# Kernel optimization log

Hardware: AMD Instinct MI355X
Metric: run time of the kernel (lower is better)

Reference implementation:

```python
import jax, jax.numpy as jnp
import numpy as np

H_SPLITS = [2, 3, 3]          # crpe_window {3:2, 5:3, 7:3}
K_SIZES = [3, 5, 7]
NUM_HEADS = 8
EPS = 1e-6


def dwconv(x, w, b, k):
    # x: (B,C,H,W), w: (C,1,k,k) depthwise, 'same' padding
    y = jax.lax.conv_general_dilated(
        x, w, (1, 1), [(k // 2, k // 2)] * 2,
        feature_group_count=x.shape[1],
        dimension_numbers=('NCHW', 'OIHW', 'NCHW'))
    return y + b[None, :, None, None]


def layernorm(x, g, b):
    m = jnp.mean(x, -1, keepdims=True)
    v = jnp.var(x, -1, keepdims=True)
    return (x - m) * jax.lax.rsqrt(v + EPS) * g + b


def conv_rel_pos_enc(q, v, ws, bs, H, W):
    # ConvRelPosEnc (MPViT style, no cls token): q * depthwise_conv(v)
    B, h, N, Ch = q.shape
    v_img = v.transpose(0, 1, 3, 2).reshape(B, h * Ch, H, W)  # B (h Ch) H W
    splits = np.cumsum([hs * Ch for hs in H_SPLITS])[:-1]
    parts = jnp.split(v_img, splits, axis=1)
    conv_v = jnp.concatenate(
        [dwconv(p, w, b, k) for p, w, b, k in zip(parts, ws, bs, K_SIZES)], axis=1)
    conv_v = conv_v.reshape(B, h, Ch, N).transpose(0, 1, 3, 2)
    return q * conv_v


def setup_inputs() -> dict:
    key = jax.random.key(0)
    B, H, W, C, nd, r, mr = 8, 64, 64, 320, 4, 2, 4
    h = NUM_HEADS
    N = H * W
    Ch = C // h
    hid = C // r
    ks = jax.random.split(key, 16)
    s = 0.02
    return {
        'x': jax.random.normal(ks[0], (B, N, C), jnp.float32),
        'domain_label': jax.nn.one_hot(jax.random.randint(ks[1], (B,), 0, nd), nd, dtype=jnp.float32),
        'cpe_w': jax.random.normal(ks[2], (C, 1, 3, 3), jnp.float32) * s,
        'cpe_b': jnp.zeros((C,), jnp.float32),
        'ln1_g': jnp.ones((C,), jnp.float32), 'ln1_b': jnp.zeros((C,), jnp.float32),
        'qkv_w': jax.random.normal(ks[3], (3 * C, C), jnp.float32) * s,
        'qkv_b': jnp.zeros((3 * C,), jnp.float32),
        'crpe_w3': jax.random.normal(ks[4], (2 * Ch, 1, 3, 3), jnp.float32) * s,
        'crpe_b3': jnp.zeros((2 * Ch,), jnp.float32),
        'crpe_w5': jax.random.normal(ks[5], (3 * Ch, 1, 5, 5), jnp.float32) * s,
        'crpe_b5': jnp.zeros((3 * Ch,), jnp.float32),
        'crpe_w7': jax.random.normal(ks[6], (3 * Ch, 1, 7, 7), jnp.float32) * s,
        'crpe_b7': jnp.zeros((3 * Ch,), jnp.float32),
        'dom_w1': jax.random.normal(ks[7], (hid, nd), jnp.float32) * s,
        'dom_b1': jnp.zeros((hid,), jnp.float32),
        'dom_w2': jax.random.normal(ks[8], (C, hid), jnp.float32) * s,
        'dom_b2': jnp.zeros((C,), jnp.float32),
        'proj_w': jax.random.normal(ks[9], (C, C), jnp.float32) * s,
        'proj_b': jnp.zeros((C,), jnp.float32),
        'ln2_g': jnp.ones((C,), jnp.float32), 'ln2_b': jnp.zeros((C,), jnp.float32),
        'mlp_w1': jax.random.normal(ks[10], (mr * C, C), jnp.float32) * s,
        'mlp_b1': jnp.zeros((mr * C,), jnp.float32),
        'mlp_w2': jax.random.normal(ks[11], (C, mr * C), jnp.float32) * s,
        'mlp_b2': jnp.zeros((C,), jnp.float32),
        'H': H, 'W': W,
    }


def reference(x, domain_label, cpe_w, cpe_b, ln1_g, ln1_b, qkv_w, qkv_b,
              crpe_w3, crpe_b3, crpe_w5, crpe_b5, crpe_w7, crpe_b7,
              dom_w1, dom_b1, dom_w2, dom_b2, proj_w, proj_b,
              ln2_g, ln2_b, mlp_w1, mlp_b1, mlp_w2, mlp_b2, H, W):
    B, N, C = x.shape
    h = NUM_HEADS
    Ch = C // h
    scale = Ch ** -0.5
    # ConvPosEnc: depthwise 3x3 conv + residual
    img = x.transpose(0, 2, 1).reshape(B, C, H, W)
    x = (dwconv(img, cpe_w, cpe_b, 3) + img).reshape(B, C, N).transpose(0, 2, 1)
    # FactorAtt_ConvRelPosEnc_Sup
    cur = layernorm(x, ln1_g, ln1_b)
    qkv = (cur @ qkv_w.T + qkv_b).reshape(B, N, 3, h, Ch).transpose(2, 0, 3, 1, 4)
    q, k, v = qkv[0], qkv[1], qkv[2]          # (B,h,N,Ch) each
    k_sm = jax.nn.softmax(k, axis=2)          # softmax over tokens
    kv = jnp.einsum('bhnk,bhnv->bhkv', k_sm, v)   # (B,h,Ch,Ch)
    fa = jnp.einsum('bhnk,bhkv->bhnv', q, kv)
    fa = scale * fa + conv_rel_pos_enc(
        q, v, (crpe_w3, crpe_w5, crpe_w7), (crpe_b3, crpe_b5, crpe_b7), H, W)
    # domain gate: MLP(one_hot) -> softmax over heads, broadcast over tokens
    d = jax.nn.relu(domain_label @ dom_w1.T + dom_b1) @ dom_w2.T + dom_b2  # (B,C)
    d = jax.nn.softmax(d.reshape(B, h, 1, Ch), axis=1)
    att = (d * fa).transpose(0, 2, 1, 3).reshape(B, N, C)
    x = x + (att @ proj_w.T + proj_b)
    # MLP (GELU, ratio 4)
    cur = layernorm(x, ln2_g, ln2_b)
    cur = jax.nn.gelu(cur @ mlp_w1.T + mlp_b1, approximate=False) @ mlp_w2.T + mlp_b2
    return x + cur
```

## Files before the change

### kernel.cpp

```cpp
#include <hip/hip_runtime.h>
#include <hip/hip_bf16.h>
#include <math.h>
#include <type_traits>

#define B_    8
#define Nn    4096
#define Cc    320
#define QS    1024
#define ATT_SCALE 0.15811388300841897f

typedef __attribute__((ext_vector_type(8))) short s8v;
typedef __attribute__((ext_vector_type(4))) float f4v;

__device__ __forceinline__ float bf2f(short u) {
    return __uint_as_float(((unsigned int)(unsigned short)u) << 16);
}
__device__ __forceinline__ short f2bf(float f) {
    return (short)__bfloat16_as_ushort(__float2bfloat16(f));
}
__device__ __forceinline__ float gelu_fast(float v) {
    float u = v * (0.7978845608f + 0.0356774081f * v * v);
    float e = __expf(2.f * u);
    float t = 1.f - 2.f / (e + 1.f);
    return 0.5f * v * (1.f + t);
}

typedef const __attribute__((address_space(1))) unsigned int* gp1_t;
typedef __attribute__((address_space(3))) unsigned int* lp3_t;
__device__ __forceinline__ void gload16(const void* g, void* l) {
    __builtin_amdgcn_global_load_lds((gp1_t)g, (lp3_t)l, 16, 0, 0);
}

__global__ void cvt_all(const float* __restrict__ s0, const float* __restrict__ s1,
                        const float* __restrict__ s2, const float* __restrict__ s3,
                        __hip_bfloat16* __restrict__ d) {
    int i = blockIdx.x * 256 + threadIdx.x;
    if (i >= 1351680) return;
    const float* s; int j, rows, K;
    if (i < 327680)      { s = s0; j = i;          rows = 960;  K = 320; }
    else if (i < 450560) { s = s1; j = i - 327680; rows = 320;  K = 320; }
    else if (i < 860160) { s = s2; j = i - 450560; rows = 1280; K = 320; }
    else                 { s = s3; j = i - 860160; rows = 320;  K = 1280; }
    float v = (j / K < rows) ? s[j] : 0.f;
    d[i] = __float2bfloat16(v);
}

template<typename T>
__global__ void ln_kernel(const T* __restrict__ x, const float* __restrict__ g,
                          const float* __restrict__ bt, __hip_bfloat16* __restrict__ out) {
    int bn = blockIdx.x;
    int lane = threadIdx.x;
    const T* row = x + (size_t)bn * Cc;
    float v[5];
    float s = 0.f, s2 = 0.f;
    #pragma unroll
    for (int i = 0; i < 5; ++i) {
        if constexpr (std::is_same<T, float>::value) v[i] = row[lane + 64 * i];
        else v[i] = bf2f(((const short*)row)[lane + 64 * i]);
        s += v[i];
        s2 += v[i] * v[i];
    }
    #pragma unroll
    for (int off = 32; off > 0; off >>= 1) {
        s  += __shfl_down(s, off);
        s2 += __shfl_down(s2, off);
    }
    s  = __shfl(s, 0);
    s2 = __shfl(s2, 0);
    float mean = s * (1.f / 320.f);
    float var  = s2 * (1.f / 320.f) - mean * mean;
    float rstd = rsqrtf(var + 1e-6f);
    __hip_bfloat16* orow = out + (size_t)bn * Cc;
    #pragma unroll
    for (int i = 0; i < 5; ++i) {
        int c = lane + 64 * i;
        orow[c] = __float2bfloat16((v[i] - mean) * rstd * g[c] + bt[c]);
    }
}

template<int ACT, int RES, int WF32, int WBF16, int KT>
__global__ __launch_bounds__(512) void gemm_mfma(
        const __hip_bfloat16* __restrict__ A, const __hip_bfloat16* __restrict__ W,
        const float* __restrict__ bias, const void* __restrict__ resv,
        float* __restrict__ outf, __hip_bfloat16* __restrict__ outb,
        int NS, int Nreal) {
    __shared__ __align__(16) short As[256 * 64];
    __shared__ __align__(16) short Bs[128 * 64];
    int tid = threadIdx.x;
    int m0 = blockIdx.x << 8;
    int n0 = blockIdx.y << 7;
    int w = tid >> 6, lane = tid & 63;
    int wr = w >> 1, wc = w & 1;
    int lrow = lane & 15, lk = lane >> 4;
    f4v acc[4][4];
    #pragma unroll
    for (int i = 0; i < 4; ++i)
        #pragma unroll
        for (int j = 0; j < 4; ++j) acc[i][j] = (f4v){0.f, 0.f, 0.f, 0.f};

    int srow = (w << 3) + (lane >> 3);
    int slot = lane & 7;

    #pragma unroll
    for (int k0 = 0; k0 < KT; k0 += 64) {
        __syncthreads();
        #pragma unroll
        for (int i = 0; i < 4; ++i) {
            int row = i * 64 + srow;
            int sk = (slot ^ (row & 7)) << 3;
            gload16(&A[(size_t)(m0 + row) * KT + k0 + sk], &As[i * 4096 + w * 512]);
        }
        #pragma unroll
        for (int i = 0; i < 2; ++i) {
            int row = i * 64 + srow;
            int sk = (slot ^ (row & 7)) << 3;
            gload16(&W[(size_t)(n0 + row) * KT + k0 + sk], &Bs[i * 4096 + w * 512]);
        }
        __syncthreads();
        #pragma unroll
        for (int ks = 0; ks < 2; ++ks) {
            s8v af[4], bf[4];
            #pragma unroll
            for (int mi = 0; mi < 4; ++mi) {
                int row = wr * 64 + mi * 16 + lrow;
                int s = (ks * 4 + lk) ^ (row & 7);
                af[mi] = *reinterpret_cast<const s8v*>(&As[row * 64 + s * 8]);
            }
            #pragma unroll
            for (int ni = 0; ni < 4; ++ni) {
                int row = wc * 64 + ni * 16 + lrow;
                int s = (ks * 4 + lk) ^ (row & 7);
                bf[ni] = *reinterpret_cast<const s8v*>(&Bs[row * 64 + s * 8]);
            }
            #pragma unroll
            for (int mi = 0; mi < 4; ++mi)
                #pragma unroll
                for (int ni = 0; ni < 4; ++ni)
                    acc[mi][ni] = __builtin_amdgcn_mfma_f32_16x16x32_bf16(bf[ni], af[mi], acc[mi][ni], 0, 0, 0);
        }
    }
    #pragma unroll
    for (int mi = 0; mi < 4; ++mi) {
        int m = m0 + wr * 64 + mi * 16 + lrow;
        #pragma unroll
        for (int ni = 0; ni < 4; ++ni) {
            int n = n0 + wc * 64 + ni * 16 + (lk << 2);
            if (n >= Nreal) continue;
            f4v v4 = acc[mi][ni];
            float4 bv = *reinterpret_cast<const float4*>(&bias[n]);
            v4[0] += bv.x; v4[1] += bv.y; v4[2] += bv.z; v4[3] += bv.w;
            if (RES == 1) {
                const float* res = (const float*)resv;
                float4 rv = *reinterpret_cast<const float4*>(&res[(size_t)m * NS + n]);
                v4[0] += rv.x; v4[1] += rv.y; v4[2] += rv.z; v4[3] += rv.w;
            } else if (RES == 2) {
                const short* res = (const short*)resv;
                short4 rv = *reinterpret_cast<const short4*>(&res[(size_t)m * NS + n]);
                v4[0] += bf2f(rv.x); v4[1] += bf2f(rv.y);
                v4[2] += bf2f(rv.z); v4[3] += bf2f(rv.w);
            }
            if (ACT == 1) {
                #pragma unroll
                for (int r = 0; r < 4; ++r) v4[r] = gelu_fast(v4[r]);
            }
            if (WF32)
                *reinterpret_cast<float4*>(&outf[(size_t)m * NS + n]) =
                    make_float4(v4[0], v4[1], v4[2], v4[3]);
            if (WBF16) {
                ushort4 u;
                u.x = (unsigned short)f2bf(v4[0]);
                u.y = (unsigned short)f2bf(v4[1]);
                u.z = (unsigned short)f2bf(v4[2]);
                u.w = (unsigned short)f2bf(v4[3]);
                *reinterpret_cast<ushort4*>(&outb[(size_t)m * NS + n]) = u;
            }
        }
    }
}

template<int KSZ, int EPI, typename ST>
__global__ __launch_bounds__(256) void dwconv_tile(
        const ST* __restrict__ src, int sstride, int scoff,
        const float* __restrict__ wts, const float* __restrict__ bias, int cbase, int ngrp,
        const void* __restrict__ aux0v,
        const float* __restrict__ aux1,
        __hip_bfloat16* __restrict__ outb) {
    constexpr int P = KSZ / 2;
    constexpr int S = 16 + 2 * P;
    __shared__ float vt[S * S * 8];
    __shared__ float ws_[8 * KSZ * KSZ];
    int blk = blockIdx.x;
    int tile = blk & 15;
    int g  = (blk >> 4) % ngrp;
    int b  = (blk >> 4) / ngrp;
    int ty0 = (tile >> 2) << 4;
    int tx0 = (tile & 3) << 4;
    int c0 = cbase + g * 8;
    int tid = threadIdx.x;
    for (int e = tid; e < 8 * KSZ * KSZ; e += 256)
        ws_[e] = wts[g * 8 * KSZ * KSZ + e];
    const ST* sb = src + (size_t)b * Nn * sstride + scoff + c0;
    for (int e = tid; e < S * S; e += 256) {
        int hy = e / S, hx = e % S;
        int gy = ty0 - P + hy, gx = tx0 - P + hx;
        float px8[8];
        #pragma unroll
        for (int j = 0; j < 8; ++j) px8[j] = 0.f;
        if ((unsigned)gy < 64u && (unsigned)gx < 64u) {
            const ST* p = &sb[(size_t)((gy << 6) + gx) * sstride];
            if constexpr (std::is_same<ST, float>::value) {
                float4 lo = reinterpret_cast<const float4*>(p)[0];
                float4 hi = reinterpret_cast<const float4*>(p)[1];
                px8[0] = lo.x; px8[1] = lo.y; px8[2] = lo.z; px8[3] = lo.w;
                px8[4] = hi.x; px8[5] = hi.y; px8[6] = hi.z; px8[7] = hi.w;
            } else {
                s8v v8 = *reinterpret_cast<const s8v*>(p);
                #pragma unroll
                for (int j = 0; j < 8; ++j) px8[j] = bf2f(v8[j]);
            }
        }
        #pragma unroll
        for (int j = 0; j < 8; ++j) vt[e * 8 + j] = px8[j];
    }
    __syncthreads();
    int cl  = tid & 7;
    int px  = (tid >> 3) & 15;
    int pyh = tid >> 7;
    int c = c0 + cl;
    float acc[8];
    float bval = bias[g * 8 + cl];
    #pragma unroll
    for (int j = 0; j < 8; ++j) acc[j] = bval;
    #pragma unroll
    for (int dx = 0; dx < KSZ; ++dx) {
        float col[8 + KSZ - 1];
        #pragma unroll
        for (int i = 0; i < 8 + KSZ - 1; ++i)
            col[i] = vt[((pyh * 8 + i) * S + (px + dx)) * 8 + cl];
        #pragma unroll
        for (int j = 0; j < 8; ++j)
            #pragma unroll
            for (int dy = 0; dy < KSZ; ++dy)
                acc[j] += col[j + dy] * ws_[cl * KSZ * KSZ + dy * KSZ + dx];
    }
    #pragma unroll
    for (int j = 0; j < 8; ++j) {
        int n = ((ty0 + pyh * 8 + j) << 6) + tx0 + px;
        size_t bn = (size_t)b * Nn + n;
        if (EPI == 0) {
            float ctr = vt[((pyh * 8 + j + P) * S + (px + P)) * 8 + cl];
            outb[bn * Cc + c] = __float2bfloat16(acc[j] + ctr);
        } else {
            const short* fa0 = (const short*)aux0v;
            float qv  = bf2f(((const short*)src)[bn * (size_t)sstride + c]);
            float fav = bf2f(fa0[bn * Cc + c]);
            float r = aux1[(size_t)b * Cc + c] * (ATT_SCALE * fav + qv * acc[j]);
            outb[bn * Cc + c] = __float2bfloat16(r);
        }
    }
}

__global__ __launch_bounds__(256) void kv_mfma(const __hip_bfloat16* __restrict__ qkv,
                                               float* __restrict__ kvp) {
    __shared__ short lds[4 * 2 * 48 * 66];
    int blk = blockIdx.x;
    int s = blk & 7;
    int bh = blk >> 3;
    int h = bh & 7, b = bh >> 3;
    int tid = threadIdx.x;
    int w = tid >> 6, lane = tid & 63;
    short* ke_t = lds + w * 2 * 48 * 66;
    short* vv_t = ke_t + 48 * 66;
    for (int e = lane; e < 8 * 66; e += 64) {
        ke_t[40 * 66 + e] = 0;
        vv_t[40 * 66 + e] = 0;
    }
    for (int n = lane; n < 66; n += 64) vv_t[40 * 66 + n] = (short)0x3F80;

    const short* kb = (const short*)qkv + (size_t)b * Nn * QS + 320 + h * 40;
    const short* vb = kb + 320;
    int col0 = lane & 15, kq = lane >> 4;
    f4v acc[3][3];
    #pragma unroll
    for (int i = 0; i < 3; ++i)
        #pragma unroll
        for (int j = 0; j < 3; ++j) acc[i][j] = (f4v){0.f, 0.f, 0.f, 0.f};

    for (int t = w; t < 8; t += 4) {
        int n0 = s * 512 + t * 64;
        for (int e = lane; e < 320; e += 64) {
            int nl = e / 5, oct = e % 5;
            size_t go = (size_t)(n0 + nl) * QS + oct * 8;
            s8v k8 = *reinterpret_cast<const s8v*>(kb + go);
            s8v v8 = *reinterpret_cast<const s8v*>(vb + go);
            #pragma unroll
            for (int j = 0; j < 8; ++j) {
                ke_t[(oct * 8 + j) * 66 + nl] = f2bf(__expf(bf2f(k8[j])));
                vv_t[(oct * 8 + j) * 66 + nl] = v8[j];
            }
        }
        __syncthreads();
        #pragma unroll
        for (int ks = 0; ks < 2; ++ks) {
            s8v af[3], bfr[3];
            #pragma unroll
            for (int mt = 0; mt < 3; ++mt)
                af[mt] = *reinterpret_cast<const s8v*>(ke_t + (mt * 16 + col0) * 66 + ks * 32 + kq * 8);
            #pragma unroll
            for (int nt = 0; nt < 3; ++nt)
                bfr[nt] = *reinterpret_cast<const s8v*>(vv_t + (nt * 16 + col0) * 66 + ks * 32 + kq * 8);
            #pragma unroll
            for (int mt = 0; mt < 3; ++mt)
                #pragma unroll
                for (int nt = 0; nt < 3; ++nt)
                    acc[mt][nt] = __builtin_amdgcn_mfma_f32_16x16x32_bf16(af[mt], bfr[nt], acc[mt][nt], 0, 0, 0);
        }
        __syncthreads();
    }
    float* red = (float*)lds;
    #pragma unroll
    for (int mt = 0; mt < 3; ++mt) {
        #pragma unroll
        for (int nt = 0; nt < 3; ++nt) {
            #pragma unroll
            for (int r = 0; r < 4; ++r) {
                int ch = mt * 16 + kq * 4 + r;
                int cv = nt * 16 + col0;
                if (ch < 40) red[w * 1920 + ch * 48 + cv] = acc[mt][nt][r];
            }
        }
    }
    __syncthreads();
    for (int p = tid; p < 1920; p += 256) {
        float sv = red[p] + red[1920 + p] + red[2 * 1920 + p] + red[3 * 1920 + p];
        kvp[(size_t)blk * 1920 + p] = sv;
    }
}

__global__ void kv_combine2(const float* __restrict__ kvp, float* __restrict__ kv) {
    int bh = blockIdx.x;
    int tid = threadIdx.x;
    __shared__ float sinv[40];
    if (tid < 40) {
        float S = 0.f;
        for (int s2 = 0; s2 < 8; ++s2)
            S += kvp[(size_t)(bh * 8 + s2) * 1920 + tid * 48 + 40];
        sinv[tid] = 1.f / S;
    }
    __syncthreads();
    for (int p = tid; p < 1600; p += 256) {
        int ch = p / 40, cv = p % 40;
        float v = 0.f;
        for (int s2 = 0; s2 < 8; ++s2)
            v += kvp[(size_t)(bh * 8 + s2) * 1920 + ch * 48 + cv];
        kv[(size_t)bh * 1600 + p] = v * sinv[ch];
    }
}

__global__ void dgate_kernel(const float* __restrict__ lbl, const float* __restrict__ w1,
                             const float* __restrict__ b1, const float* __restrict__ w2,
                             const float* __restrict__ b2, float* __restrict__ dg) {
    int b = blockIdx.x;
    int tid = threadIdx.x;
    __shared__ float hid[160];
    __shared__ float dd[320];
    if (tid < 160) {
        float a = b1[tid];
        for (int d = 0; d < 4; ++d) a += w1[tid * 4 + d] * lbl[b * 4 + d];
        hid[tid] = fmaxf(a, 0.f);
    }
    __syncthreads();
    float a = b2[tid];
    for (int j = 0; j < 160; ++j) a += w2[tid * 160 + j] * hid[j];
    dd[tid] = a;
    __syncthreads();
    if (tid < 40) {
        float M = -1e30f;
        for (int h2 = 0; h2 < 8; ++h2) M = fmaxf(M, dd[h2 * 40 + tid]);
        float S = 0.f;
        float e[8];
        for (int h2 = 0; h2 < 8; ++h2) { e[h2] = __expf(dd[h2 * 40 + tid] - M); S += e[h2]; }
        float inv = 1.f / S;
        for (int h2 = 0; h2 < 8; ++h2) dg[b * 320 + h2 * 40 + tid] = e[h2] * inv;
    }
}

__global__ __launch_bounds__(256) void fa_kernel(const __hip_bfloat16* __restrict__ qkv,
        const float* __restrict__ kvmat, __hip_bfloat16* __restrict__ fa) {
    __shared__ float kvs[1600];
    int blk = blockIdx.x;
    int chunk = blk & 15;
    int bh = blk >> 4;
    int h = bh & 7, b = bh >> 3;
    int tid = threadIdx.x;
    for (int e = tid; e < 1600; e += 256) kvs[e] = kvmat[(size_t)bh * 1600 + e];
    __syncthreads();
    int n = chunk * 256 + tid;
    const short* qr = (const short*)qkv + (size_t)(b * Nn + n) * QS + h * 40;
    float q[40];
    #pragma unroll
    for (int i = 0; i < 5; ++i) {
        s8v v8 = reinterpret_cast<const s8v*>(qr)[i];
        #pragma unroll
        for (int j = 0; j < 8; ++j) q[i * 8 + j] = bf2f(v8[j]);
    }
    float o[40];
    #pragma unroll
    for (int cv = 0; cv < 40; ++cv) o[cv] = 0.f;
    #pragma unroll
    for (int ch = 0; ch < 40; ++ch) {
        float qv = q[ch];
        #pragma unroll
        for (int cv = 0; cv < 40; ++cv)
            o[cv] += qv * kvs[ch * 40 + cv];
    }
    short* fr = (short*)fa + (size_t)(b * Nn + n) * 320 + h * 40;
    #pragma unroll
    for (int i = 0; i < 5; ++i) {
        s8v u;
        #pragma unroll
        for (int j = 0; j < 8; ++j) u[j] = f2bf(o[i * 8 + j]);
        *reinterpret_cast<s8v*>(fr + i * 8) = u;
    }
}

extern "C" void kernel_launch(void* const* d_in, const int* in_sizes, int n_in,
                              void* d_out, int out_size, void* d_ws, size_t ws_size,
                              hipStream_t stream) {
    const float* x     = (const float*)d_in[0];
    const float* lbl   = (const float*)d_in[1];
    const float* cpe_w = (const float*)d_in[2];
    const float* cpe_b = (const float*)d_in[3];
    const float* ln1g  = (const float*)d_in[4];
    const float* ln1b  = (const float*)d_in[5];
    const float* qkv_w = (const float*)d_in[6];
    const float* qkv_b = (const float*)d_in[7];
    const float* w3    = (const float*)d_in[8];
    const float* b3    = (const float*)d_in[9];
    const float* w5    = (const float*)d_in[10];
    const float* b5    = (const float*)d_in[11];
    const float* w7    = (const float*)d_in[12];
    const float* b7    = (const float*)d_in[13];
    const float* dw1   = (const float*)d_in[14];
    const float* db1   = (const float*)d_in[15];
    const float* dw2   = (const float*)d_in[16];
    const float* db2   = (const float*)d_in[17];
    const float* pw    = (const float*)d_in[18];
    const float* pb    = (const float*)d_in[19];
    const float* ln2g  = (const float*)d_in[20];
    const float* ln2b  = (const float*)d_in[21];
    const float* m1w   = (const float*)d_in[22];
    const float* m1b   = (const float*)d_in[23];
    const float* m2w   = (const float*)d_in[24];
    const float* m2b   = (const float*)d_in[25];
    float* out = (float*)d_out;

    float* ws = (float*)d_ws;
    __hip_bfloat16* x1b  = (__hip_bfloat16*)ws; ws += 5242880;
    __hip_bfloat16* qkvb = (__hip_bfloat16*)ws; ws += 16777216;
    float* big  = ws; ws += 20971520;
    __hip_bfloat16* gelub = (__hip_bfloat16*)big;
    __hip_bfloat16* fab   = (__hip_bfloat16*)ws; ws += 5242880;
    __hip_bfloat16* bb1   = (__hip_bfloat16*)ws; ws += 5242880;
    __hip_bfloat16* wb    = (__hip_bfloat16*)ws; ws += 675840;
    float* kvp  = ws; ws += 983040;
    float* kv   = ws; ws += 102400;
    float* dg   = ws; ws += 2560;
    __hip_bfloat16* wbq  = wb;
    __hip_bfloat16* wbp  = wbq  + 1024 * 320;
    __hip_bfloat16* wbm1 = wbp  + 384 * 320;
    __hip_bfloat16* wbm2 = wbm1 + 1280 * 320;

    cvt_all<<<5280, 256, 0, stream>>>(qkv_w, pw, m1w, m2w, wb);
    dwconv_tile<3, 0, float><<<B_ * 40 * 16, 256, 0, stream>>>(
        x, 320, 0, cpe_w, cpe_b, 0, 40, nullptr, nullptr, x1b);
    ln_kernel<__hip_bfloat16><<<B_ * Nn, 64, 0, stream>>>(x1b, ln1g, ln1b, bb1);
    {
        dim3 g(128, 8);
        gemm_mfma<0, 0, 0, 1, 320><<<g, 512, 0, stream>>>(bb1, wbq, qkv_b, nullptr,
                                                          nullptr, qkvb, QS, 960);
    }
    kv_mfma<<<512, 256, 0, stream>>>(qkvb, kvp);
    kv_combine2<<<64, 256, 0, stream>>>(kvp, kv);
    dgate_kernel<<<B_, 320, 0, stream>>>(lbl, dw1, db1, dw2, db2, dg);
    fa_kernel<<<B_ * 8 * 16, 256, 0, stream>>>(qkvb, kv, fab);
    dwconv_tile<3, 1, __hip_bfloat16><<<B_ * 10 * 16, 256, 0, stream>>>(
        qkvb, QS, 640, w3, b3, 0, 10, fab, dg, bb1);
    dwconv_tile<5, 1, __hip_bfloat16><<<B_ * 15 * 16, 256, 0, stream>>>(
        qkvb, QS, 640, w5, b5, 80, 15, fab, dg, bb1);
    dwconv_tile<7, 1, __hip_bfloat16><<<B_ * 15 * 16, 256, 0, stream>>>(
        qkvb, QS, 640, w7, b7, 200, 15, fab, dg, bb1);
    {
        dim3 g(128, 3);
        gemm_mfma<0, 2, 1, 0, 320><<<g, 512, 0, stream>>>(bb1, wbp, pb, x1b,
                                                          out, nullptr, 320, 320);
    }
    ln_kernel<float><<<B_ * Nn, 64, 0, stream>>>(out, ln2g, ln2b, bb1);
    {
        dim3 g(128, 10);
        gemm_mfma<1, 0, 0, 1, 320><<<g, 512, 0, stream>>>(bb1, wbm1, m1b, nullptr,
                                                          nullptr, gelub, 1280, 1280);
    }
    {
        dim3 g(128, 3);
        gemm_mfma<0, 1, 1, 0, 1280><<<g, 512, 0, stream>>>(gelub, wbm2, m2b, out,
                                                           out, nullptr, 320, 320);
    }
}
```

Measured before the change: 315.3 us.

## Add full-N GEMM kernel for N=320 outputs and grouped block swizzle

Adds a gemm_fulln kernel with a 64-row by full-320-column tile for the projection and MLP2 GEMMs. This removes the padded 384-column tiling and the wasted third N-tile, and raises the block count to 512. The main GEMM now uses a 1D grid with a grouped swizzle (8 M-tiles per group) so that blocks sharing A tiles run close together for better L2 reuse. In exchange, the smaller M tile reuses each W load across fewer rows, and more of the W matrix is staged per block.

```diff
diff --git a/kernel.cpp b/kernel.cpp
--- a/kernel.cpp
+++ b/kernel.cpp
@@ -83,12 +83,15 @@
         const __hip_bfloat16* __restrict__ A, const __hip_bfloat16* __restrict__ W,
         const float* __restrict__ bias, const void* __restrict__ resv,
         float* __restrict__ outf, __hip_bfloat16* __restrict__ outb,
-        int NS, int Nreal) {
+        int NS, int Nreal, int gy) {
     __shared__ __align__(16) short As[256 * 64];
     __shared__ __align__(16) short Bs[128 * 64];
-    int tid = threadIdx.x;
-    int m0 = blockIdx.x << 8;
-    int n0 = blockIdx.y << 7;
+    int bid = blockIdx.x;
+    int grp8 = gy << 3;
+    int grp = bid / grp8, rem = bid % grp8;
+    int m0 = ((grp << 3) + (rem & 7)) << 8;
+    int n0 = (rem >> 3) << 7;
+    int tid = threadIdx.x;
     int w = tid >> 6, lane = tid & 63;
     int wr = w >> 1, wc = w & 1;
     int lrow = lane & 15, lk = lane >> 4;
@@ -146,6 +149,102 @@
         for (int ni = 0; ni < 4; ++ni) {
             int n = n0 + wc * 64 + ni * 16 + (lk << 2);
             if (n >= Nreal) continue;
+            f4v v4 = acc[mi][ni];
+            float4 bv = *reinterpret_cast<const float4*>(&bias[n]);
+            v4[0] += bv.x; v4[1] += bv.y; v4[2] += bv.z; v4[3] += bv.w;
+            if (RES == 1) {
+                const float* res = (const float*)resv;
+                float4 rv = *reinterpret_cast<const float4*>(&res[(size_t)m * NS + n]);
+                v4[0] += rv.x; v4[1] += rv.y; v4[2] += rv.z; v4[3] += rv.w;
+            } else if (RES == 2) {
+                const short* res = (const short*)resv;
+                short4 rv = *reinterpret_cast<const short4*>(&res[(size_t)m * NS + n]);
+                v4[0] += bf2f(rv.x); v4[1] += bf2f(rv.y);
+                v4[2] += bf2f(rv.z); v4[3] += bf2f(rv.w);
+            }
+            if (ACT == 1) {
+                #pragma unroll
+                for (int r = 0; r < 4; ++r) v4[r] = gelu_fast(v4[r]);
+            }
+            if (WF32)
+                *reinterpret_cast<float4*>(&outf[(size_t)m * NS + n]) =
+                    make_float4(v4[0], v4[1], v4[2], v4[3]);
+            if (WBF16) {
+                ushort4 u;
+                u.x = (unsigned short)f2bf(v4[0]);
+                u.y = (unsigned short)f2bf(v4[1]);
+                u.z = (unsigned short)f2bf(v4[2]);
+                u.w = (unsigned short)f2bf(v4[3]);
+                *reinterpret_cast<ushort4*>(&outb[(size_t)m * NS + n]) = u;
+            }
+        }
+    }
+}
+
+template<int ACT, int RES, int WF32, int WBF16, int KT>
+__global__ __launch_bounds__(512) void gemm_fulln(
+        const __hip_bfloat16* __restrict__ A, const __hip_bfloat16* __restrict__ W,
+        const float* __restrict__ bias, const void* __restrict__ resv,
+        float* __restrict__ outf, __hip_bfloat16* __restrict__ outb,
+        int NS) {
+    __shared__ __align__(16) short As[64 * 64];
+    __shared__ __align__(16) short Ws[320 * 64];
+    int tid = threadIdx.x;
+    int m0 = blockIdx.x << 6;
+    int w = tid >> 6, lane = tid & 63;
+    int wr = w >> 2, wc = w & 3;
+    int lrow = lane & 15, lk = lane >> 4;
+    f4v acc[2][5];
+    #pragma unroll
+    for (int i = 0; i < 2; ++i)
+        #pragma unroll
+        for (int j = 0; j < 5; ++j) acc[i][j] = (f4v){0.f, 0.f, 0.f, 0.f};
+
+    int srow = tid >> 3;
+    int slot = tid & 7;
+
+    #pragma unroll
+    for (int k0 = 0; k0 < KT; k0 += 64) {
+        __syncthreads();
+        {
+            int sk = (slot ^ (srow & 7)) << 3;
+            gload16(&A[(size_t)(m0 + srow) * KT + k0 + sk], &As[w * 512]);
+        }
+        #pragma unroll
+        for (int i = 0; i < 5; ++i) {
+            int row = i * 64 + srow;
+            int sk = (slot ^ (row & 7)) << 3;
+            gload16(&W[(size_t)row * KT + k0 + sk], &Ws[i * 4096 + w * 512]);
+        }
+        __syncthreads();
+        #pragma unroll
+        for (int ks = 0; ks < 2; ++ks) {
+            s8v af[2], bf[5];
+            #pragma unroll
+            for (int mi = 0; mi < 2; ++mi) {
+                int row = wr * 32 + mi * 16 + lrow;
+                int s = (ks * 4 + lk) ^ (row & 7);
+                af[mi] = *reinterpret_cast<const s8v*>(&As[row * 64 + s * 8]);
+            }
+            #pragma unroll
+            for (int ni = 0; ni < 5; ++ni) {
+                int row = wc * 80 + ni * 16 + lrow;
+                int s = (ks * 4 + lk) ^ (row & 7);
+                bf[ni] = *reinterpret_cast<const s8v*>(&Ws[row * 64 + s * 8]);
+            }
+            #pragma unroll
+            for (int mi = 0; mi < 2; ++mi)
+                #pragma unroll
+                for (int ni = 0; ni < 5; ++ni)
+                    acc[mi][ni] = __builtin_amdgcn_mfma_f32_16x16x32_bf16(bf[ni], af[mi], acc[mi][ni], 0, 0, 0);
+        }
+    }
+    #pragma unroll
+    for (int mi = 0; mi < 2; ++mi) {
+        int m = m0 + wr * 32 + mi * 16 + lrow;
+        #pragma unroll
+        for (int ni = 0; ni < 5; ++ni) {
+            int n = wc * 80 + ni * 16 + (lk << 2);
             f4v v4 = acc[mi][ni];
             float4 bv = *reinterpret_cast<const float4*>(&bias[n]);
             v4[0] += bv.x; v4[1] += bv.y; v4[2] += bv.z; v4[3] += bv.w;
@@ -475,11 +574,8 @@
     dwconv_tile<3, 0, float><<<B_ * 40 * 16, 256, 0, stream>>>(
         x, 320, 0, cpe_w, cpe_b, 0, 40, nullptr, nullptr, x1b);
     ln_kernel<__hip_bfloat16><<<B_ * Nn, 64, 0, stream>>>(x1b, ln1g, ln1b, bb1);
-    {
-        dim3 g(128, 8);
-        gemm_mfma<0, 0, 0, 1, 320><<<g, 512, 0, stream>>>(bb1, wbq, qkv_b, nullptr,
-                                                          nullptr, qkvb, QS, 960);
-    }
+    gemm_mfma<0, 0, 0, 1, 320><<<1024, 512, 0, stream>>>(bb1, wbq, qkv_b, nullptr,
+                                                         nullptr, qkvb, QS, 960, 8);
     kv_mfma<<<512, 256, 0, stream>>>(qkvb, kvp);
     kv_combine2<<<64, 256, 0, stream>>>(kvp, kv);
     dgate_kernel<<<B_, 320, 0, stream>>>(lbl, dw1, db1, dw2, db2, dg);
@@ -490,20 +586,11 @@
         qkvb, QS, 640, w5, b5, 80, 15, fab, dg, bb1);
     dwconv_tile<7, 1, __hip_bfloat16><<<B_ * 15 * 16, 256, 0, stream>>>(
         qkvb, QS, 640, w7, b7, 200, 15, fab, dg, bb1);
-    {
-        dim3 g(128, 3);
-        gemm_mfma<0, 2, 1, 0, 320><<<g, 512, 0, stream>>>(bb1, wbp, pb, x1b,
-                                                          out, nullptr, 320, 320);
-    }
+    gemm_fulln<0, 2, 1, 0, 320><<<512, 512, 0, stream>>>(bb1, wbp, pb, x1b,
+                                                         out, nullptr, 320);
     ln_kernel<float><<<B_ * Nn, 64, 0, stream>>>(out, ln2g, ln2b, bb1);
-    {
-        dim3 g(128, 10);
-        gemm_mfma<1, 0, 0, 1, 320><<<g, 512, 0, stream>>>(bb1, wbm1, m1b, nullptr,
-                                                          nullptr, gelub, 1280, 1280);
-    }
-    {
-        dim3 g(128, 3);
-        gemm_mfma<0, 1, 1, 0, 1280><<<g, 512, 0, stream>>>(gelub, wbm2, m2b, out,
-                                                           out, nullptr, 320, 320);
-    }
-}
+    gemm_mfma<1, 0, 0, 1, 320><<<1280, 512, 0, stream>>>(bb1, wbm1, m1b, nullptr,
+                                                         nullptr, gelub, 1280, 1280, 10);
+    gemm_fulln<0, 1, 1, 0, 1280><<<512, 512, 0, stream>>>(gelub, wbm2, m2b, out,
+                                                          out, nullptr, 320);
+}
```

After: 310.0 us. Within noise of the previous version (-1.7%).
